# Optimization experiments

Hardware: AMD Instinct MI355X
Metric: run time of the kernel (lower is better)

## Reference

```python
import jax, jax.numpy as jnp
import numpy as np

NUM_HEADS = 4

def setup_inputs() -> dict:
    key = jax.random.key(0)
    ks = jax.random.split(key, 7)
    B, Lq, Lk, E, D, LAT = 16, 256, 4096, 64, 32, 32
    query = jax.random.normal(ks[0], (B, Lq, E), dtype=jnp.float32)
    key_in = jax.random.normal(ks[1], (B, Lk, E), dtype=jnp.float32)
    value = jax.random.normal(ks[2], (B, Lk, D), dtype=jnp.float32)
    mask = jax.random.randint(ks[3], (B, Lk, D), 0, 2, dtype=jnp.int32)
    Wq = jax.random.normal(ks[4], (E, E), dtype=jnp.float32) / np.sqrt(E).astype(np.float32)
    bq = jnp.zeros((E,), dtype=jnp.float32)
    Wk = jax.random.normal(ks[5], (E, E), dtype=jnp.float32) / np.sqrt(E).astype(np.float32)
    bk = jnp.zeros((E,), dtype=jnp.float32)
    Wo = jax.random.normal(ks[6], (NUM_HEADS * D, LAT), dtype=jnp.float32) / np.sqrt(NUM_HEADS * D).astype(np.float32)
    bo = jnp.zeros((LAT,), dtype=jnp.float32)
    return {"query": query, "key": key_in, "value": value, "mask": mask,
            "Wq": Wq, "bq": bq, "Wk": Wk, "bk": bk, "Wo": Wo, "bo": bo}

def reference(query, key, value, mask, Wq, bq, Wk, bk, Wo, bo):
    B, Lk, D = value.shape
    Lq = query.shape[1]
    h = NUM_HEADS
    ek = query.shape[-1] // h  # embed_time_k
    # linear maps (torch Linear: y = x @ W; here W stored as (in, out))
    q = (query @ Wq + bq).reshape(B, Lq, h, ek).transpose(0, 2, 1, 3)  # (B,h,Lq,ek)
    k = (key @ Wk + bk).reshape(B, Lk, h, ek).transpose(0, 2, 1, 3)    # (B,h,Lk,ek)
    scores = jnp.einsum('bhqe,bhke->bhqk', q, k) / jnp.sqrt(jnp.asarray(ek, q.dtype))
    # Original repeats scores over D, masks per-feature with -inf, softmaxes over Lk,
    # then does a weighted sum. Equivalent fused form (never builds (B,h,Lq,Lk,D)):
    e = jnp.exp(scores - jnp.max(scores, axis=-1, keepdims=True))  # (B,h,Lq,Lk)
    m = mask.astype(value.dtype)                                   # (B,Lk,D) 0/1
    num = jnp.einsum('bhqk,bkd->bhqd', e, m * value)
    den = jnp.einsum('bhqk,bkd->bhqd', e, m)
    x = num / den                                                  # (B,h,Lq,D)
    x = x.transpose(0, 2, 1, 3).reshape(B, Lq, h * D)
    return x @ Wo + bo  # (B, Lq, latent_dim)
```

## Files before the change

kernel.cpp:

```cpp
#include <hip/hip_runtime.h>
#include <hip/hip_bf16.h>
#include <math.h>

typedef __bf16 bf16;
typedef bf16 bf16x4 __attribute__((ext_vector_type(4)));
typedef bf16 bf16x8 __attribute__((ext_vector_type(8)));
typedef float f32x4 __attribute__((ext_vector_type(4)));

#define B_   16
#define LQ_  256
#define LK_  4096
#define E_   64
#define H_   4
#define EK_  16
#define D_   32
#define LAT_ 32

#define OFF_QP    0u
#define OFF_KP    524288u
#define OFF_MVFB  8912896u
#define OFF_WOT   17301504u
#define WS_NEED   17309696u

#define LOG2E 1.44269504f

__device__ inline f32x4 mfma_bf16(bf16x8 a, bf16x8 b, f32x4 c) {
  return __builtin_amdgcn_mfma_f32_16x16x32_bf16(a, b, c, 0, 0, 0);
}
__device__ inline bf16x8 zero8() {
  bf16x8 z;
#pragma unroll
  for (int i = 0; i < 8; ++i) z[i] = (bf16)0.0f;
  return z;
}

__global__ __launch_bounds__(256) void prep_kernel(
    const float* __restrict__ query, const float* __restrict__ key,
    const float* __restrict__ value, const int* __restrict__ mask,
    const float* __restrict__ Wq, const float* __restrict__ bq,
    const float* __restrict__ Wk, const float* __restrict__ bk,
    const float* __restrict__ Wo,
    bf16* __restrict__ qp, bf16* __restrict__ kp,
    bf16* __restrict__ mvfB, bf16* __restrict__ WoT)
{
  __shared__ __align__(16) bf16 s_b[16896];
  const int bid = blockIdx.x;
  const int tid = threadIdx.x;

  if (bid < 544) {
    const bool isQ = bid < 32;
    const int row0 = isQ ? bid * 128 : (bid - 32) * 128;
    const float* in   = isQ ? query : key;
    const float* W    = isQ ? Wq : Wk;
    const float* bias = isQ ? bq : bk;
    bf16* outp        = isQ ? qp : kp;
    const float scal  = isQ ? (0.25f * LOG2E) : 1.0f;

    bf16* sIn = s_b;
    bf16* sWT = s_b + 9216;

#pragma unroll
    for (int p = 0; p < 8; ++p) {
      int f4 = tid + p * 256;
      int row = f4 >> 4, e4 = (f4 & 15) * 4;
      float4 v = *(const float4*)(in + (size_t)(row0 + row) * 64 + e4);
      bf16x4 b4;
      b4[0] = (bf16)v.x; b4[1] = (bf16)v.y; b4[2] = (bf16)v.z; b4[3] = (bf16)v.w;
      *(bf16x4*)(sIn + row * 72 + e4) = b4;
    }
#pragma unroll
    for (int p = 0; p < 4; ++p) {
      int f4 = tid + p * 256;
      int k = f4 >> 4, c4 = (f4 & 15) * 4;
      float4 v = *(const float4*)(W + k * 64 + c4);
      sWT[(c4 + 0) * 72 + k] = (bf16)v.x;
      sWT[(c4 + 1) * 72 + k] = (bf16)v.y;
      sWT[(c4 + 2) * 72 + k] = (bf16)v.z;
      sWT[(c4 + 3) * 72 + k] = (bf16)v.w;
    }
    __syncthreads();

    const int w = tid >> 6, l = tid & 63, l15 = l & 15, g = l >> 4;
    f32x4 acc[2][4];
#pragma unroll
    for (int mt = 0; mt < 2; ++mt)
#pragma unroll
      for (int nt = 0; nt < 4; ++nt) acc[mt][nt] = f32x4{0.f, 0.f, 0.f, 0.f};

#pragma unroll
    for (int ks = 0; ks < 2; ++ks) {
      bf16x8 A0 = *(bf16x8*)(sIn + (32 * w + l15) * 72 + 32 * ks + 8 * g);
      bf16x8 A1 = *(bf16x8*)(sIn + (32 * w + 16 + l15) * 72 + 32 * ks + 8 * g);
#pragma unroll
      for (int nt = 0; nt < 4; ++nt) {
        bf16x8 Bf = *(bf16x8*)(sWT + (16 * nt + l15) * 72 + 32 * ks + 8 * g);
        acc[0][nt] = mfma_bf16(A0, Bf, acc[0][nt]);
        acc[1][nt] = mfma_bf16(A1, Bf, acc[1][nt]);
      }
    }
#pragma unroll
    for (int mt = 0; mt < 2; ++mt)
#pragma unroll
      for (int nt = 0; nt < 4; ++nt) {
        int col = 16 * nt + l15;
        float bv = bias[col];
#pragma unroll
        for (int r = 0; r < 4; ++r) {
          int row = row0 + 32 * w + 16 * mt + 4 * g + r;
          outp[(size_t)row * 64 + col] = (bf16)((acc[mt][nt][r] + bv) * scal);
        }
      }
  } else if (bid < 800) {
    const int rb = bid - 544;
    const int b = rb >> 4, kk0 = (rb & 15) * 256;
#pragma unroll
    for (int p = 0; p < 8; ++p) {
      int f4 = tid + p * 256;
      int kk = f4 >> 3, d4 = (f4 & 7) * 4;
      size_t gi = ((size_t)(b * LK_ + kk0 + kk)) * 32 + d4;
      float4 v = *(const float4*)(value + gi);
      int4   m = *(const int4*)(mask + gi);
      s_b[(d4 + 0) * 264 + kk] = (bf16)(m.x ? v.x : 0.0f);
      s_b[(d4 + 1) * 264 + kk] = (bf16)(m.y ? v.y : 0.0f);
      s_b[(d4 + 2) * 264 + kk] = (bf16)(m.z ? v.z : 0.0f);
      s_b[(d4 + 3) * 264 + kk] = (bf16)(m.w ? v.w : 0.0f);
      s_b[(32 + d4 + 0) * 264 + kk] = (bf16)(float)m.x;
      s_b[(32 + d4 + 1) * 264 + kk] = (bf16)(float)m.y;
      s_b[(32 + d4 + 2) * 264 + kk] = (bf16)(float)m.z;
      s_b[(32 + d4 + 3) * 264 + kk] = (bf16)(float)m.w;
    }
    __syncthreads();
    const int col = tid >> 2, seg = tid & 3;
    const int nt = col >> 4, l15c = col & 15;
#pragma unroll
    for (int w2 = 0; w2 < 8; ++w2) {
      int kkg = seg * 64 + w2 * 8;
      int tile = (kk0 + kkg) >> 5;
      int gq = (kkg >> 3) & 3;
      int lane = 16 * gq + l15c;
      uint4 d = *(uint4*)(s_b + col * 264 + kkg);
      *(uint4*)(mvfB + (size_t)((((b * 128 + tile) * 4 + nt) * 64 + lane)) * 8) = d;
    }
  } else {
#pragma unroll
    for (int p = 0; p < 16; ++p) {
      int f = tid + p * 256;
      int k = f >> 5, n = f & 31;
      WoT[n * 128 + k] = (bf16)Wo[f];
    }
  }
}

__global__ __launch_bounds__(512, 2) void fused_attn(
    const bf16* __restrict__ qp, const bf16* __restrict__ kp,
    const bf16* __restrict__ mvfB, const bf16* __restrict__ WoT,
    const float* __restrict__ bo, float* __restrict__ out)
{
  __shared__ __align__(16) bf16  s_se[8 * 640];
  __shared__ __align__(16) float s_acc[4 * 16 * 65];
  __shared__ __align__(16) bf16  s_x[16 * 136];

  const int bid = blockIdx.x;
  const int b = bid >> 4, qt = bid & 15;
  const int q0 = qt * 16;
  const int tid = threadIdx.x;
  const int w = tid >> 6, l = tid & 63, l15 = l & 15, g = l >> 4;
  const int h = w & 3, s = w >> 2;
  const int tile0 = s * 64;

  bf16x8 qB;
  if (l < 32) {
    qB = *(const bf16x8*)(qp + (size_t)((b * LQ_ + q0 + l15) * 64 + h * EK_ + g * 8));
  } else { qB = zero8(); }

  f32x4 acc[4];
#pragma unroll
  for (int nt = 0; nt < 4; ++nt) acc[nt] = f32x4{0.f, 0.f, 0.f, 0.f};

  bf16* se_w = s_se + w * 640;
  const bf16* mvt0 = mvfB + (size_t)(b * 128 + tile0) * 2048;
  const bf16* kp_b = kp + (size_t)(b * LK_ + tile0 * 32) * 64 + h * EK_ + g * 8;

#pragma unroll 2
  for (int t = 0; t < 64; ++t) {
    const bf16* mvt = mvt0 + (size_t)t * 2048;

    bf16x8 mvB[4];
#pragma unroll
    for (int nt = 0; nt < 4; ++nt)
      mvB[nt] = *(const bf16x8*)(mvt + (nt * 64 + l) * 8);

    bf16x8 kA0, kA1;
    if (l < 32) {
      kA0 = *(const bf16x8*)(kp_b + (size_t)(t * 32 + l15) * 64);
      kA1 = *(const bf16x8*)(kp_b + (size_t)(t * 32 + 16 + l15) * 64);
    } else { kA0 = zero8(); kA1 = zero8(); }

    f32x4 S0 = mfma_bf16(kA0, qB, f32x4{0.f, 0.f, 0.f, 0.f});
    f32x4 S1 = mfma_bf16(kA1, qB, f32x4{0.f, 0.f, 0.f, 0.f});

    bf16x4 e0, e1;
#pragma unroll
    for (int r = 0; r < 4; ++r) { e0[r] = (bf16)exp2f(S0[r]); e1[r] = (bf16)exp2f(S1[r]); }
    *(bf16x4*)(se_w + l15 * 40 + 4 * g)      = e0;
    *(bf16x4*)(se_w + l15 * 40 + 16 + 4 * g) = e1;

    asm volatile("" ::: "memory");

    bf16x8 eA = *(bf16x8*)(se_w + l15 * 40 + 8 * g);

#pragma unroll
    for (int nt = 0; nt < 4; ++nt)
      acc[nt] = mfma_bf16(eA, mvB[nt], acc[nt]);
  }

  if (s == 1) {
    float* pa = s_acc + h * 1040;
#pragma unroll
    for (int nt = 0; nt < 4; ++nt)
#pragma unroll
      for (int r = 0; r < 4; ++r)
        pa[(4 * g + r) * 65 + 16 * nt + l15] = acc[nt][r];
  }
  __syncthreads();
  if (s == 0) {
    const float* pa = s_acc + h * 1040;
#pragma unroll
    for (int nt = 0; nt < 2; ++nt)
#pragma unroll
      for (int r = 0; r < 4; ++r) {
        int q = 4 * g + r, dcol = 16 * nt + l15;
        float num = acc[nt][r]     + pa[q * 65 + dcol];
        float den = acc[nt + 2][r] + pa[q * 65 + dcol + 32];
        s_x[q * 136 + h * 32 + dcol] = (bf16)(num / den);
      }
  }
  __syncthreads();
  if (w < 2) {
    const int nt = w;
    f32x4 oacc = f32x4{0.f, 0.f, 0.f, 0.f};
#pragma unroll
    for (int ks = 0; ks < 4; ++ks) {
      bf16x8 A  = *(bf16x8*)(s_x + l15 * 136 + 32 * ks + 8 * g);
      bf16x8 Bf = *(const bf16x8*)(WoT + (l15 + 16 * nt) * 128 + 32 * ks + 8 * g);
      oacc = mfma_bf16(A, Bf, oacc);
    }
    float bv = bo[l15 + 16 * nt];
#pragma unroll
    for (int r = 0; r < 4; ++r) {
      int row = q0 + 4 * g + r;
      out[(size_t)(b * LQ_ + row) * LAT_ + l15 + 16 * nt] = oacc[r] + bv;
    }
  }
}

extern "C" void kernel_launch(void* const* d_in, const int* in_sizes, int n_in,
                              void* d_out, int out_size, void* d_ws, size_t ws_size,
                              hipStream_t stream) {
  const float* query = (const float*)d_in[0];
  const float* key   = (const float*)d_in[1];
  const float* value = (const float*)d_in[2];
  const int*   mask  = (const int*)d_in[3];
  const float* Wq    = (const float*)d_in[4];
  const float* bq    = (const float*)d_in[5];
  const float* Wk    = (const float*)d_in[6];
  const float* bk    = (const float*)d_in[7];
  const float* Wo    = (const float*)d_in[8];
  const float* bo    = (const float*)d_in[9];
  float* out = (float*)d_out;
  char* ws = (char*)d_ws;

  if (ws_size < (size_t)WS_NEED) return;

  bf16* qp   = (bf16*)(ws + OFF_QP);
  bf16* kp   = (bf16*)(ws + OFF_KP);
  bf16* mvfB = (bf16*)(ws + OFF_MVFB);
  bf16* WoT  = (bf16*)(ws + OFF_WOT);

  prep_kernel<<<801, 256, 0, stream>>>(query, key, value, mask, Wq, bq, Wk, bk,
                                       Wo, qp, kp, mvfB, WoT);
  fused_attn<<<256, 512, 0, stream>>>(qp, kp, mvfB, WoT, bo, out);
}
```

Before: 131.5 us.

## Split attention over key chunks into partial buffers and add reduction kernel

The fused attention kernel, which used 256 blocks each splitting Lk across two wave groups, becomes a split-K kernel with 2048 blocks of 256 threads. Each block handles one eighth of the key range and writes fp32 partial numerator and denominator sums to a workspace buffer. A new output kernel adds the eight partials, divides, and applies the Wo projection. This raises occupancy and parallelism across the GPU's CUs, at the cost of an extra launch and about 33 MB of partial-sum traffic through global memory.

```diff
diff --git a/kernel.cpp b/kernel.cpp
--- a/kernel.cpp
+++ b/kernel.cpp
@@ -20,7 +20,8 @@
 #define OFF_KP    524288u
 #define OFF_MVFB  8912896u
 #define OFF_WOT   17301504u
-#define WS_NEED   17309696u
+#define OFF_NDP   17309696u
+#define WS_NEED   50864128u
 
 #define LOG2E 1.44269504f
 
@@ -151,22 +152,18 @@
   }
 }
 
-__global__ __launch_bounds__(512, 2) void fused_attn(
+__global__ __launch_bounds__(256, 8) void attn_kernel(
     const bf16* __restrict__ qp, const bf16* __restrict__ kp,
-    const bf16* __restrict__ mvfB, const bf16* __restrict__ WoT,
-    const float* __restrict__ bo, float* __restrict__ out)
+    const bf16* __restrict__ mvfB, float* __restrict__ ndp)
 {
-  __shared__ __align__(16) bf16  s_se[8 * 640];
-  __shared__ __align__(16) float s_acc[4 * 16 * 65];
-  __shared__ __align__(16) bf16  s_x[16 * 136];
+  __shared__ __align__(16) bf16 s_se[4 * 640];
 
   const int bid = blockIdx.x;
-  const int b = bid >> 4, qt = bid & 15;
+  const int kc = bid & 7, qt = (bid >> 3) & 15, b = bid >> 7;
+  const int tid = threadIdx.x;
+  const int h = tid >> 6, l = tid & 63, l15 = l & 15, g = l >> 4;
   const int q0 = qt * 16;
-  const int tid = threadIdx.x;
-  const int w = tid >> 6, l = tid & 63, l15 = l & 15, g = l >> 4;
-  const int h = w & 3, s = w >> 2;
-  const int tile0 = s * 64;
+  const int tile0 = kc * 16;
 
   bf16x8 qB;
   if (l < 32) {
@@ -177,12 +174,12 @@
 #pragma unroll
   for (int nt = 0; nt < 4; ++nt) acc[nt] = f32x4{0.f, 0.f, 0.f, 0.f};
 
-  bf16* se_w = s_se + w * 640;
+  bf16* se_w = s_se + h * 640;
   const bf16* mvt0 = mvfB + (size_t)(b * 128 + tile0) * 2048;
   const bf16* kp_b = kp + (size_t)(b * LK_ + tile0 * 32) * 64 + h * EK_ + g * 8;
 
 #pragma unroll 2
-  for (int t = 0; t < 64; ++t) {
+  for (int t = 0; t < 16; ++t) {
     const bf16* mvt = mvt0 + (size_t)t * 2048;
 
     bf16x8 mvB[4];
@@ -214,42 +211,60 @@
       acc[nt] = mfma_bf16(eA, mvB[nt], acc[nt]);
   }
 
-  if (s == 1) {
-    float* pa = s_acc + h * 1040;
-#pragma unroll
-    for (int nt = 0; nt < 4; ++nt)
-#pragma unroll
-      for (int r = 0; r < 4; ++r)
-        pa[(4 * g + r) * 65 + 16 * nt + l15] = acc[nt][r];
+  float* ndp_w = ndp + ((((size_t)kc * B_ + b) * H_ + h) * LQ_) * 64;
+#pragma unroll
+  for (int nt = 0; nt < 4; ++nt)
+#pragma unroll
+    for (int r = 0; r < 4; ++r) {
+      int q = q0 + 4 * g + r;
+      int col = 16 * nt + l15;
+      ndp_w[(size_t)q * 64 + col] = acc[nt][r];
+    }
+}
+
+__global__ __launch_bounds__(256) void out_kernel(
+    const float* __restrict__ ndp, const bf16* __restrict__ WoT,
+    const float* __restrict__ bo, float* __restrict__ out)
+{
+  __shared__ __align__(16) bf16 s_x[16 * 136];
+  const int bid = blockIdx.x;
+  const int b = bid >> 4, q0 = (bid & 15) * 16;
+  const int tid = threadIdx.x;
+  const int q = tid >> 4, jg = tid & 15;
+  const int h = jg >> 2, d0 = (jg & 3) * 8;
+
+  f32x4 nlo = f32x4{0.f,0.f,0.f,0.f}, nhi = f32x4{0.f,0.f,0.f,0.f};
+  f32x4 dlo = f32x4{0.f,0.f,0.f,0.f}, dhi = f32x4{0.f,0.f,0.f,0.f};
+#pragma unroll
+  for (int kc = 0; kc < 8; ++kc) {
+    const float* p = ndp + ((((size_t)kc * B_ + b) * H_ + h) * LQ_ + q0 + q) * 64;
+    nlo += *(const f32x4*)(p + d0);
+    nhi += *(const f32x4*)(p + d0 + 4);
+    dlo += *(const f32x4*)(p + 32 + d0);
+    dhi += *(const f32x4*)(p + 32 + d0 + 4);
+  }
+  bf16* sx = s_x + q * 136 + h * 32 + d0;
+#pragma unroll
+  for (int i = 0; i < 4; ++i) {
+    sx[i]     = (bf16)(nlo[i] / dlo[i]);
+    sx[4 + i] = (bf16)(nhi[i] / dhi[i]);
   }
   __syncthreads();
-  if (s == 0) {
-    const float* pa = s_acc + h * 1040;
-#pragma unroll
-    for (int nt = 0; nt < 2; ++nt)
-#pragma unroll
-      for (int r = 0; r < 4; ++r) {
-        int q = 4 * g + r, dcol = 16 * nt + l15;
-        float num = acc[nt][r]     + pa[q * 65 + dcol];
-        float den = acc[nt + 2][r] + pa[q * 65 + dcol + 32];
-        s_x[q * 136 + h * 32 + dcol] = (bf16)(num / den);
-      }
-  }
-  __syncthreads();
+  const int w = tid >> 6, l = tid & 63, l15 = l & 15, g = l >> 4;
   if (w < 2) {
     const int nt = w;
-    f32x4 oacc = f32x4{0.f, 0.f, 0.f, 0.f};
+    f32x4 acc = f32x4{0.f, 0.f, 0.f, 0.f};
 #pragma unroll
     for (int ks = 0; ks < 4; ++ks) {
       bf16x8 A  = *(bf16x8*)(s_x + l15 * 136 + 32 * ks + 8 * g);
       bf16x8 Bf = *(const bf16x8*)(WoT + (l15 + 16 * nt) * 128 + 32 * ks + 8 * g);
-      oacc = mfma_bf16(A, Bf, oacc);
+      acc = mfma_bf16(A, Bf, acc);
     }
     float bv = bo[l15 + 16 * nt];
 #pragma unroll
     for (int r = 0; r < 4; ++r) {
       int row = q0 + 4 * g + r;
-      out[(size_t)(b * LQ_ + row) * LAT_ + l15 + 16 * nt] = oacc[r] + bv;
+      out[(size_t)(b * LQ_ + row) * LAT_ + l15 + 16 * nt] = acc[r] + bv;
     }
   }
 }
@@ -276,8 +291,10 @@
   bf16* kp   = (bf16*)(ws + OFF_KP);
   bf16* mvfB = (bf16*)(ws + OFF_MVFB);
   bf16* WoT  = (bf16*)(ws + OFF_WOT);
+  float* ndp = (float*)(ws + OFF_NDP);
 
   prep_kernel<<<801, 256, 0, stream>>>(query, key, value, mask, Wq, bq, Wk, bk,
                                        Wo, qp, kp, mvfB, WoT);
-  fused_attn<<<256, 512, 0, stream>>>(qp, kp, mvfB, WoT, bo, out);
-}
+  attn_kernel<<<2048, 256, 0, stream>>>(qp, kp, mvfB, ndp);
+  out_kernel<<<256, 256, 0, stream>>>(ndp, WoT, bo, out);
+}
```

Result: slower. 140.6 us (+7.0%).
